# Performance work log

Measured on AMD Instinct MI355X. Metric: run time of the kernel, lower is better.

## Reference

```python
import jax, jax.numpy as jnp
import numpy as np

H = 8  # n_heads


def setup_inputs() -> dict:
    key = jax.random.key(0)
    ks = jax.random.split(key, 14)
    B, Lq, Lk, D = 8, 1024, 1024, 512  # batch, query len, kv len, in_dim
    d = 512                            # per-head out dim (out_dim before *= n_heads)
    s = 0.02                           # weight init scale
    x = jax.random.normal(ks[0], (B, Lq, D), jnp.float32)
    y = jax.random.normal(ks[1], (B, Lk, D), jnp.float32)
    x_pos = jax.random.normal(ks[2], (B, Lq, D), jnp.float32)
    y_pos = jax.random.normal(ks[3], (B, Lk, D), jnp.float32)
    x_mask = jnp.ones((B, Lq), dtype=bool)
    y_mask = jax.random.randint(ks[4], (B, Lk), 0, 2).astype(bool)
    Wq = jax.random.normal(ks[5], (H * d, D), jnp.float32) * s
    bq = jax.random.normal(ks[6], (H * d,), jnp.float32) * s
    Wk = jax.random.normal(ks[7], (H * d, D), jnp.float32) * s
    bk = jax.random.normal(ks[8], (H * d,), jnp.float32) * s
    Wv = jax.random.normal(ks[9], (H * d, D), jnp.float32) * s
    bv = jax.random.normal(ks[10], (H * d,), jnp.float32) * s
    Wp = jax.random.normal(ks[11], (d, D), jnp.float32) * s  # residual projection, no bias
    gamma = jax.random.uniform(ks[12], (H, 1, 1, 1), jnp.float32) + 0.001
    return dict(x=x, y=y, x_mask=x_mask, y_mask=y_mask, x_pos=x_pos, y_pos=y_pos,
                Wq=Wq, bq=bq, Wk=Wk, bk=bk, Wv=Wv, bv=bv, Wp=Wp, gamma=gamma)


def reference(x, y, x_mask, y_mask, x_pos, y_pos, Wq, bq, Wk, bk, Wv, bv, Wp, gamma):
    B, Lq, D = x.shape
    nH = gamma.shape[0]
    # QKV projections; query/key use positional-augmented inputs (with_pose)
    q = (x + x_pos) @ Wq.T + bq            # [B, Lq, H*d]
    k = (y + y_pos) @ Wk.T + bk            # [B, Lk, H*d]
    v = y @ Wv.T + bv                      # [B, Lk, H*d]
    d = q.shape[-1] // nH

    def heads(t):
        # split_cat: split last dim into H chunks, stack as leading head dim -> [H, B, L, d]
        return t.reshape(B, -1, nH, d).transpose(2, 0, 1, 3)

    qh, kh, vh = heads(q), heads(k), heads(v)
    # Unscaled attention energy (module applies no 1/sqrt(d) scaling)
    energy = jnp.einsum('hbqd,hbkd->hbqk', qh, kh)     # [H, B, Lq, Lk]
    mask = x_mask[:, :, None] & y_mask[:, None, :]     # [B, Lq, Lk]
    energy = jnp.where(mask[None], energy, -jnp.inf)
    attn = jax.nn.softmax(energy, axis=-1)
    out = jnp.einsum('hbqk,hbkd->hbqd', attn, vh)      # [H, B, Lq, d]
    # Gated residual: project x to per-head dim, blend with learnable gamma
    xp = x @ Wp.T                                      # [B, Lq, d]
    out = (gamma * out + xp[None]) / (gamma + 1.0)
    return out.transpose(1, 0, 2, 3)                   # [B, H, Lq, d]
```

## Files before the change

kernel.cpp:

```cpp
#include <hip/hip_runtime.h>


typedef __attribute__((ext_vector_type(8))) short short8;
typedef __attribute__((ext_vector_type(4))) float f32x4;
typedef __attribute__((ext_vector_type(4))) unsigned short ushort4v;

__device__ __forceinline__ unsigned short f2bf(float f) {
  unsigned int u = __builtin_bit_cast(unsigned int, f);
  u = (u + 0x7fffu + ((u >> 16) & 1u)) >> 16;
  return (unsigned short)u;
}

__device__ __forceinline__ f32x4 mfma16(short8 a, short8 b, f32x4 c) {
  return __builtin_amdgcn_mfma_f32_16x16x32_bf16(a, b, c, 0, 0, 0);
}

__device__ __forceinline__ void gld16(void* l, const void* g) {
  __builtin_amdgcn_global_load_lds(
      (const __attribute__((address_space(1))) unsigned int*)(unsigned long long)(__SIZE_TYPE__)g,
      (__attribute__((address_space(3))) unsigned int*)(unsigned int)(__SIZE_TYPE__)l,
      16, 0, 0);
}


__global__ void detect_mask_kernel(const void* __restrict__ ym, int* __restrict__ flag) {
  __shared__ int bad_i, bad_f;
  if (threadIdx.x == 0) { bad_i = 0; bad_f = 0; }
  __syncthreads();
  const int* ip = (const int*)ym;
  const float* fp = (const float*)ym;
  for (int i = threadIdx.x; i < 2048; i += 256) {
    int v = ip[i];
    if (v != 0 && v != 1) bad_i = 1;
    float f = fp[i];
    if (!(f == 0.0f || f == 1.0f)) bad_f = 1;
  }
  __syncthreads();
  if (threadIdx.x == 0) *flag = bad_i ? (bad_f ? 0 : 2) : 1;
}

__global__ __launch_bounds__(256) void conv_add2(const float* __restrict__ a,
                                                 const float* __restrict__ b,
                                                 unsigned short* __restrict__ o) {
  size_t base = ((size_t)blockIdx.x * 256 + threadIdx.x) * 8;
  f32x4 v0 = *(const f32x4*)(a + base), v1 = *(const f32x4*)(a + base + 4);
  f32x4 u0 = *(const f32x4*)(b + base), u1 = *(const f32x4*)(b + base + 4);
  v0 += u0; v1 += u1;
  short8 sv;
#pragma unroll
  for (int e = 0; e < 4; e++) { sv[e] = (short)f2bf(v0[e]); sv[4 + e] = (short)f2bf(v1[e]); }
  *(short8*)(o + base) = sv;
}

__global__ __launch_bounds__(256) void conv1(const float* __restrict__ a,
                                             unsigned short* __restrict__ o) {
  size_t base = ((size_t)blockIdx.x * 256 + threadIdx.x) * 8;
  f32x4 v0 = *(const f32x4*)(a + base), v1 = *(const f32x4*)(a + base + 4);
  short8 sv;
#pragma unroll
  for (int e = 0; e < 4; e++) { sv[e] = (short)f2bf(v0[e]); sv[4 + e] = (short)f2bf(v1[e]); }
  *(short8*)(o + base) = sv;
}

template<int STAGE, int BIASF, int MODE>
__global__ __launch_bounds__(256, 2) void gemm_k512(
    const void* __restrict__ Av, const void* __restrict__ Bv,
    const float* __restrict__ bias, void* __restrict__ out, int N)
{
  constexpr int K = 512;
  __shared__ unsigned short As[2][128][64];
  __shared__ unsigned short Bs[2][128][64];
  const int tid = threadIdx.x;
  const int w = tid >> 6, lane = tid & 63, g = lane >> 4, r16 = lane & 15;
  const int nwg = gridDim.x, flat = blockIdx.x;
  const int swz = (flat & 7) * (nwg >> 3) + (flat >> 3);
  const int m0 = (swz & 63) * 128, n0 = (swz >> 6) * 128;
  const int mblk = (w & 1) * 64, nblk = (w >> 1) * 64;

  auto stage = [&](int bb, int k0) {
    if (STAGE == 0) {
      const unsigned short* Ab = (const unsigned short*)Av;
      const unsigned short* Bb = (const unsigned short*)Bv;
#pragma unroll
      for (int i = 0; i < 4; i++) {
        int row0 = (w * 4 + i) * 8;
        int row = row0 + (lane >> 3), c = (lane & 7) ^ (row & 7);
        gld16(&As[bb][row0][0], Ab + (size_t)(m0 + row) * K + k0 + c * 8);
      }
#pragma unroll
      for (int i = 0; i < 4; i++) {
        int row0 = (w * 4 + i) * 8;
        int row = row0 + (lane >> 3), c = (lane & 7) ^ (row & 7);
        gld16(&Bs[bb][row0][0], Bb + (size_t)(n0 + row) * K + k0 + c * 8);
      }
    } else {
      const float* Af = (const float*)Av;
      const float* Bf = (const float*)Bv;
#pragma unroll
      for (int c = 0; c < 4; c++) {
        int fl = c * 256 + tid, row = fl >> 3, c8 = fl & 7;
        const float* px = Af + (size_t)(m0 + row) * K + k0 + c8 * 8;
        f32x4 v0 = *(const f32x4*)px, v1 = *(const f32x4*)(px + 4);
        short8 sv;
#pragma unroll
        for (int e = 0; e < 4; e++) { sv[e] = (short)f2bf(v0[e]); sv[4 + e] = (short)f2bf(v1[e]); }
        *(short8*)&As[bb][row][(c8 ^ (row & 7)) * 8] = sv;
      }
#pragma unroll
      for (int c = 0; c < 4; c++) {
        int fl = c * 256 + tid, row = fl >> 3, c8 = fl & 7;
        const float* pw = Bf + (size_t)(n0 + row) * K + k0 + c8 * 8;
        f32x4 v0 = *(const f32x4*)pw, v1 = *(const f32x4*)(pw + 4);
        short8 sv;
#pragma unroll
        for (int e = 0; e < 4; e++) { sv[e] = (short)f2bf(v0[e]); sv[4 + e] = (short)f2bf(v1[e]); }
        *(short8*)&Bs[bb][row][(c8 ^ (row & 7)) * 8] = sv;
      }
    }
  };

  f32x4 acc[4][4];
#pragma unroll
  for (int i = 0; i < 4; i++)
#pragma unroll
    for (int j = 0; j < 4; j++) acc[i][j] = f32x4{0.f, 0.f, 0.f, 0.f};

  stage(0, 0);
  __syncthreads();

  for (int t = 0; t < 8; t++) {
    const int cur = t & 1;
    if (t < 7) stage(cur ^ 1, (t + 1) * 64);
#pragma unroll
    for (int kk = 0; kk < 2; kk++) {
      short8 af[4], bfv[4];
#pragma unroll
      for (int mt = 0; mt < 4; mt++)
        af[mt] = *(const short8*)&As[cur][mblk + mt * 16 + r16][(((kk * 4 + g)) ^ (r16 & 7)) * 8];
#pragma unroll
      for (int nt = 0; nt < 4; nt++)
        bfv[nt] = *(const short8*)&Bs[cur][nblk + nt * 16 + r16][(((kk * 4 + g)) ^ (r16 & 7)) * 8];
#pragma unroll
      for (int mt = 0; mt < 4; mt++)
#pragma unroll
        for (int nt = 0; nt < 4; nt++)
          acc[mt][nt] = mfma16(af[mt], bfv[nt], acc[mt][nt]);
    }
    __syncthreads();
  }

#pragma unroll
  for (int nt = 0; nt < 4; nt++) {
    int n_g = n0 + nblk + nt * 16 + r16;
    float bval = BIASF ? bias[n_g] : 0.0f;
#pragma unroll
    for (int mt = 0; mt < 4; mt++) {
      int row4 = m0 + mblk + mt * 16 + g * 4;
      if (MODE == 1) {
        int bB = row4 >> 10, tok = row4 & 1023, hh = n_g >> 9, dh = n_g & 511;
        int t32 = tok & ~31, a = (tok & 31) >> 2;
        int ptok = t32 + ((a & 3) << 3) + ((a >> 2) << 2);
        ushort4v pk;
#pragma unroll
        for (int r = 0; r < 4; r++) pk[r] = f2bf(acc[mt][nt][r] + bval);
        *(ushort4v*)((unsigned short*)out + ((size_t)(bB * 8 + hh) * 512 + dh) * 1024 + ptok) = pk;
      } else if (MODE == 0) {
#pragma unroll
        for (int r = 0; r < 4; r++)
          ((unsigned short*)out)[(size_t)(row4 + r) * N + n_g] = f2bf(acc[mt][nt][r] + bval);
      } else {
#pragma unroll
        for (int r = 0; r < 4; r++)
          ((float*)out)[(size_t)(row4 + r) * N + n_g] = acc[mt][nt][r] + bval;
      }
    }
  }
}

__global__ __launch_bounds__(512, 2) void attn_kernel(
    const unsigned short* __restrict__ qptr, const unsigned short* __restrict__ kptr,
    const unsigned short* __restrict__ vtptr, const float* __restrict__ xpptr,
    const void* __restrict__ ymask, const int* __restrict__ mflag,
    const float* __restrict__ gamma, float* __restrict__ outp)
{
  __shared__ unsigned short Ks[2][32][512];
  __shared__ unsigned short Vs[2][512][32];
  __shared__ float mb[1024];

  int flat = blockIdx.y * 8 + blockIdx.x;
  int wg = (flat & 7) * 64 + (flat >> 3);
  int bh = wg >> 3, qt = wg & 7;
  int b = bh >> 3, h = bh & 7;
  int q0 = qt * 128;
  const int tid = threadIdx.x, w = tid >> 6, lane = tid & 63, g = lane >> 4, r16 = lane & 15;
  const int fm = *mflag;

  for (int i = tid; i < 1024; i += 512) {
    int keyg = b * 1024 + i;
    bool valid;
    if (fm == 1)      valid = ((const int*)ymask)[keyg] != 0;
    else if (fm == 2) valid = ((const float*)ymask)[keyg] != 0.0f;
    else              valid = ((const unsigned char*)ymask)[keyg] != 0;
    mb[i] = valid ? 0.0f : -2e30f;
  }

  const unsigned short* kbase = kptr + (size_t)(b * 1024) * 4096 + h * 512;
  const unsigned short* vbase = vtptr + (size_t)(bh * 512) * 1024;

  short8 qf[16];
  {
    const unsigned short* qrow = qptr + (size_t)(b * 1024 + q0 + w * 16 + r16) * 4096 + h * 512;
#pragma unroll
    for (int kk = 0; kk < 16; kk++) qf[kk] = *(const short8*)(qrow + kk * 32 + g * 8);
  }

  f32x4 o[32];
#pragma unroll
  for (int i = 0; i < 32; i++) o[i] = f32x4{0.f, 0.f, 0.f, 0.f};
  float m_run = -1e30f, l_run = 0.0f;

#pragma unroll
  for (int i = 0; i < 4; i++) {
    int r = w * 4 + i;
    gld16(&Ks[0][r][0], kbase + (size_t)r * 4096 + ((unsigned)(lane ^ (r & 7)) << 3));
  }
#pragma unroll
  for (int j = 0; j < 4; j++) {
    int dim0 = w * 64 + j * 16;
    gld16(&Vs[0][dim0][0], vbase + (size_t)(dim0 + (lane >> 2)) * 1024 + (lane & 3) * 8);
  }
  __syncthreads();

  for (int kt = 0; kt < 32; kt++) {
    const int cur = kt & 1, nxt = cur ^ 1;
    if (kt < 31) {
#pragma unroll
      for (int i = 0; i < 4; i++) {
        int r = w * 4 + i;
        gld16(&Ks[nxt][r][0],
              kbase + (size_t)((kt + 1) * 32 + r) * 4096 + ((unsigned)(lane ^ (r & 7)) << 3));
      }
#pragma unroll
      for (int j = 0; j < 4; j++) {
        int dim0 = w * 64 + j * 16;
        gld16(&Vs[nxt][dim0][0],
              vbase + (size_t)(dim0 + (lane >> 2)) * 1024 + (kt + 1) * 32 + (lane & 3) * 8);
      }
    }

    f32x4 s0a = f32x4{0.f,0.f,0.f,0.f}, s0b = f32x4{0.f,0.f,0.f,0.f};
    f32x4 s1a = f32x4{0.f,0.f,0.f,0.f}, s1b = f32x4{0.f,0.f,0.f,0.f};
    __builtin_amdgcn_s_setprio(1);
#pragma unroll
    for (int kk = 0; kk < 16; kk += 2) {
      short8 a0 = *(const short8*)&Ks[cur][r16][((kk * 4 + g) ^ (r16 & 7)) * 8];
      short8 a1 = *(const short8*)&Ks[cur][16 + r16][((kk * 4 + g) ^ (r16 & 7)) * 8];
      s0a = mfma16(a0, qf[kk], s0a);
      s1a = mfma16(a1, qf[kk], s1a);
      short8 c0 = *(const short8*)&Ks[cur][r16][(((kk + 1) * 4 + g) ^ (r16 & 7)) * 8];
      short8 c1 = *(const short8*)&Ks[cur][16 + r16][(((kk + 1) * 4 + g) ^ (r16 & 7)) * 8];
      s0b = mfma16(c0, qf[kk + 1], s0b);
      s1b = mfma16(c1, qf[kk + 1], s1b);
    }
    __builtin_amdgcn_s_setprio(0);
    f32x4 s0 = s0a + s0b, s1 = s1a + s1b;

    int kb = kt * 32 + 4 * g;
#pragma unroll
    for (int r = 0; r < 4; r++) { s0[r] += mb[kb + r]; s1[r] += mb[kb + 16 + r]; }

    float mx = fmaxf(fmaxf(fmaxf(s0[0], s0[1]), fmaxf(s0[2], s0[3])),
                     fmaxf(fmaxf(s1[0], s1[1]), fmaxf(s1[2], s1[3])));
    mx = fmaxf(mx, __shfl_xor(mx, 16));
    mx = fmaxf(mx, __shfl_xor(mx, 32));
    float mn = fmaxf(m_run, mx);
    float alpha = __expf(m_run - mn);
    m_run = mn;
    float p0[4], p1[4], sum = 0.0f;
#pragma unroll
    for (int r = 0; r < 4; r++) {
      p0[r] = (s0[r] < -1e29f) ? 0.0f : __expf(s0[r] - mn);
      p1[r] = (s1[r] < -1e29f) ? 0.0f : __expf(s1[r] - mn);
      sum += p0[r] + p1[r];
    }
    sum += __shfl_xor(sum, 16);
    sum += __shfl_xor(sum, 32);
    l_run = l_run * alpha + sum;

    if (!__all(alpha == 1.0f)) {
      float ao[4];
#pragma unroll
      for (int r = 0; r < 4; r++)
        ao[r] = __shfl(alpha, (lane & 48) | (4 * ((lane >> 4) & 3) + r));
#pragma unroll
      for (int nt = 0; nt < 32; nt++)
#pragma unroll
        for (int r = 0; r < 4; r++) o[nt][r] *= ao[r];
    }

    short8 pa;
#pragma unroll
    for (int e = 0; e < 4; e++) { pa[e] = (short)f2bf(p0[e]); pa[4 + e] = (short)f2bf(p1[e]); }

    __builtin_amdgcn_s_setprio(1);
#pragma unroll
    for (int nt = 0; nt < 32; nt++) {
      short8 bv = *(const short8*)&Vs[cur][nt * 16 + r16][g * 8];
      o[nt] = mfma16(pa, bv, o[nt]);
    }
    __builtin_amdgcn_s_setprio(0);
    __syncthreads();
  }

  float il[4];
#pragma unroll
  for (int r = 0; r < 4; r++)
    il[r] = 1.0f / __shfl(l_run, (lane & 48) | (4 * ((lane >> 4) & 3) + r));
  float gm = gamma[h];
  float c1 = gm / (gm + 1.0f), c2 = 1.0f / (gm + 1.0f);
#pragma unroll
  for (int nt = 0; nt < 32; nt++) {
    int dim = nt * 16 + r16;
#pragma unroll
    for (int r = 0; r < 4; r++) {
      int qrow = q0 + w * 16 + g * 4 + r;
      float xv = xpptr[(size_t)(b * 1024 + qrow) * 512 + dim];
      outp[((size_t)(b * 8 + h) * 1024 + qrow) * 512 + dim] = c1 * (o[nt][r] * il[r]) + c2 * xv;
    }
  }
}

extern "C" void kernel_launch(void* const* d_in, const int* in_sizes, int n_in,
                              void* d_out, int out_size, void* d_ws, size_t ws_size,
                              hipStream_t stream) {
  (void)in_sizes; (void)n_in; (void)out_size; (void)ws_size;
  const float* x     = (const float*)d_in[0];
  const float* y     = (const float*)d_in[1];
  const void*  ymask = d_in[3];
  const float* xpos  = (const float*)d_in[4];
  const float* ypos  = (const float*)d_in[5];
  const float* Wq    = (const float*)d_in[6];
  const float* bq    = (const float*)d_in[7];
  const float* Wk    = (const float*)d_in[8];
  const float* bk    = (const float*)d_in[9];
  const float* Wv    = (const float*)d_in[10];
  const float* bv    = (const float*)d_in[11];
  const float* Wp    = (const float*)d_in[12];
  const float* gamma = (const float*)d_in[13];

  char* ws = (char*)d_ws;
  unsigned short* q_ws  = (unsigned short*)(ws);
  unsigned short* k_ws  = (unsigned short*)(ws + (64ul << 20));
  unsigned short* xqb   = (unsigned short*)(ws + (64ul << 20));
  unsigned short* Wqb   = (unsigned short*)(ws + (72ul << 20));
  unsigned short* vt_ws = (unsigned short*)(ws + (128ul << 20));
  unsigned short* ykb   = (unsigned short*)(ws + (128ul << 20));
  unsigned short* Wkb   = (unsigned short*)(ws + (136ul << 20));
  unsigned short* xb    = (unsigned short*)(ws + (140ul << 20));
  unsigned short* Wpb   = (unsigned short*)(ws + (148ul << 20));
  float*          xp_ws = (float*)(ws + (192ul << 20));
  int*            flag  = (int*)(ws + (208ul << 20));

  detect_mask_kernel<<<1, 256, 0, stream>>>(ymask, flag);
  conv_add2<<<2048, 256, 0, stream>>>(x, xpos, xqb);
  conv1<<<1024, 256, 0, stream>>>(Wq, Wqb);
  conv_add2<<<2048, 256, 0, stream>>>(y, ypos, ykb);
  conv1<<<1024, 256, 0, stream>>>(Wk, Wkb);
  conv1<<<2048, 256, 0, stream>>>(x, xb);
  conv1<<<128, 256, 0, stream>>>(Wp, Wpb);

  gemm_k512<0, 1, 0><<<2048, 256, 0, stream>>>(xqb, Wqb, bq, q_ws, 4096);
  gemm_k512<0, 0, 2><<<256, 256, 0, stream>>>(xb, Wpb, nullptr, xp_ws, 512);
  gemm_k512<0, 1, 0><<<2048, 256, 0, stream>>>(ykb, Wkb, bk, k_ws, 4096);
  gemm_k512<1, 1, 1><<<2048, 256, 0, stream>>>(y, Wv, bv, vt_ws, 4096);

  attn_kernel<<<dim3(8, 64), 512, 0, stream>>>(q_ws, k_ws, vt_ws, xp_ws, ymask, flag,
                                               gamma, (float*)d_out);
}
```

Measured before the change: 574.5 us.

## Swizzle V tile in LDS, lazy softmax rescale, pre-convert V-projection inputs to bf16

XOR-swizzles the V^T tile layout in shared memory so the PV-stage reads avoid bank conflicts. The online softmax now rescales the output accumulators only when the new row max exceeds the running max by more than 8, so most tiles skip the 128-register rescale, at the cost of larger exponent headroom. The masked-key select is dropped because exp of a -2e30 bias already gives zero. When the workspace is large enough, y and Wv are converted to bf16 beforehand so the V GEMM uses the bf16 input path instead of converting fp32 on the fly, adding two conversion launches.

After: 550.7 us. -4.1%, faster.

```diff
diff --git a/kernel.cpp b/kernel.cpp
--- a/kernel.cpp
+++ b/kernel.cpp
@@ -205,7 +205,7 @@
   }
 
   const unsigned short* kbase = kptr + (size_t)(b * 1024) * 4096 + h * 512;
-  const unsigned short* vbase = vtptr + (size_t)(bh * 512) * 1024;
+  const unsigned short* vbase = vtptr + (size_t)bh * 512 * 1024;
 
   short8 qf[16];
   {
@@ -227,7 +227,9 @@
 #pragma unroll
   for (int j = 0; j < 4; j++) {
     int dim0 = w * 64 + j * 16;
-    gld16(&Vs[0][dim0][0], vbase + (size_t)(dim0 + (lane >> 2)) * 1024 + (lane & 3) * 8);
+    int drow = dim0 + (lane >> 2);
+    int p = (lane & 3) ^ ((drow >> 1) & 3);
+    gld16(&Vs[0][dim0][0], vbase + (size_t)drow * 1024 + p * 8);
   }
   __syncthreads();
 
@@ -243,8 +245,9 @@
 #pragma unroll
       for (int j = 0; j < 4; j++) {
         int dim0 = w * 64 + j * 16;
-        gld16(&Vs[nxt][dim0][0],
-              vbase + (size_t)(dim0 + (lane >> 2)) * 1024 + (kt + 1) * 32 + (lane & 3) * 8);
+        int drow = dim0 + (lane >> 2);
+        int p = (lane & 3) ^ ((drow >> 1) & 3);
+        gld16(&Vs[nxt][dim0][0], vbase + (size_t)drow * 1024 + (kt + 1) * 32 + p * 8);
       }
     }
 
@@ -273,30 +276,33 @@
                      fmaxf(fmaxf(s1[0], s1[1]), fmaxf(s1[2], s1[3])));
     mx = fmaxf(mx, __shfl_xor(mx, 16));
     mx = fmaxf(mx, __shfl_xor(mx, 32));
-    float mn = fmaxf(m_run, mx);
-    float alpha = __expf(m_run - mn);
-    m_run = mn;
+    float mn;
+    if (__all(mx - m_run <= 8.0f)) {
+      mn = m_run;
+    } else {
+      mn = fmaxf(m_run, mx);
+      float alpha = __expf(m_run - mn);
+      m_run = mn;
+      float ao[4];
+#pragma unroll
+      for (int r = 0; r < 4; r++)
+        ao[r] = __shfl(alpha, (lane & 48) | (4 * ((lane >> 4) & 3) + r));
+#pragma unroll
+      for (int nt = 0; nt < 32; nt++)
+#pragma unroll
+        for (int r = 0; r < 4; r++) o[nt][r] *= ao[r];
+      l_run *= alpha;
+    }
     float p0[4], p1[4], sum = 0.0f;
 #pragma unroll
     for (int r = 0; r < 4; r++) {
-      p0[r] = (s0[r] < -1e29f) ? 0.0f : __expf(s0[r] - mn);
-      p1[r] = (s1[r] < -1e29f) ? 0.0f : __expf(s1[r] - mn);
+      p0[r] = __expf(s0[r] - mn);
+      p1[r] = __expf(s1[r] - mn);
       sum += p0[r] + p1[r];
     }
     sum += __shfl_xor(sum, 16);
     sum += __shfl_xor(sum, 32);
-    l_run = l_run * alpha + sum;
-
-    if (!__all(alpha == 1.0f)) {
-      float ao[4];
-#pragma unroll
-      for (int r = 0; r < 4; r++)
-        ao[r] = __shfl(alpha, (lane & 48) | (4 * ((lane >> 4) & 3) + r));
-#pragma unroll
-      for (int nt = 0; nt < 32; nt++)
-#pragma unroll
-        for (int r = 0; r < 4; r++) o[nt][r] *= ao[r];
-    }
+    l_run += sum;
 
     short8 pa;
 #pragma unroll
@@ -305,7 +311,8 @@
     __builtin_amdgcn_s_setprio(1);
 #pragma unroll
     for (int nt = 0; nt < 32; nt++) {
-      short8 bv = *(const short8*)&Vs[cur][nt * 16 + r16][g * 8];
+      int row = nt * 16 + r16;
+      short8 bv = *(const short8*)&Vs[cur][row][(g ^ ((row >> 1) & 3)) * 8];
       o[nt] = mfma16(pa, bv, o[nt]);
     }
     __builtin_amdgcn_s_setprio(0);
@@ -333,7 +340,7 @@
 extern "C" void kernel_launch(void* const* d_in, const int* in_sizes, int n_in,
                               void* d_out, int out_size, void* d_ws, size_t ws_size,
                               hipStream_t stream) {
-  (void)in_sizes; (void)n_in; (void)out_size; (void)ws_size;
+  (void)in_sizes; (void)n_in; (void)out_size;
   const float* x     = (const float*)d_in[0];
   const float* y     = (const float*)d_in[1];
   const void*  ymask = d_in[3];
@@ -360,6 +367,9 @@
   unsigned short* Wpb   = (unsigned short*)(ws + (148ul << 20));
   float*          xp_ws = (float*)(ws + (192ul << 20));
   int*            flag  = (int*)(ws + (208ul << 20));
+  unsigned short* yb    = (unsigned short*)(ws + (209ul << 20));
+  unsigned short* Wvb   = (unsigned short*)(ws + (217ul << 20));
+  const bool big = ws_size >= (221ul << 20);
 
   detect_mask_kernel<<<1, 256, 0, stream>>>(ymask, flag);
   conv_add2<<<2048, 256, 0, stream>>>(x, xpos, xqb);
@@ -368,11 +378,18 @@
   conv1<<<1024, 256, 0, stream>>>(Wk, Wkb);
   conv1<<<2048, 256, 0, stream>>>(x, xb);
   conv1<<<128, 256, 0, stream>>>(Wp, Wpb);
+  if (big) {
+    conv1<<<2048, 256, 0, stream>>>(y, yb);
+    conv1<<<1024, 256, 0, stream>>>(Wv, Wvb);
+  }
 
   gemm_k512<0, 1, 0><<<2048, 256, 0, stream>>>(xqb, Wqb, bq, q_ws, 4096);
   gemm_k512<0, 0, 2><<<256, 256, 0, stream>>>(xb, Wpb, nullptr, xp_ws, 512);
   gemm_k512<0, 1, 0><<<2048, 256, 0, stream>>>(ykb, Wkb, bk, k_ws, 4096);
-  gemm_k512<1, 1, 1><<<2048, 256, 0, stream>>>(y, Wv, bv, vt_ws, 4096);
+  if (big)
+    gemm_k512<0, 1, 1><<<2048, 256, 0, stream>>>(yb, Wvb, bv, vt_ws, 4096);
+  else
+    gemm_k512<1, 1, 1><<<2048, 256, 0, stream>>>(y, Wv, bv, vt_ws, 4096);
 
   attn_kernel<<<dim3(8, 64), 512, 0, stream>>>(q_ws, k_ws, vt_ws, xp_ws, ymask, flag,
                                                gamma, (float*)d_out);
```
